# Performance work log

Hardware: AMD Instinct MI355X
Metric: run time of the kernel (lower is better)

Reference implementation:

```python
import jax, jax.numpy as jnp
import numpy as np

B, N, D, H = 4, 1024, 512, 8
DH = D // H  # per-head dim for V and for each of the two Q/K halves
LAM = 0.5


def setup_inputs() -> dict:
    key = jax.random.key(0)
    ks = jax.random.split(key, 7)
    s = 0.02
    return {
        "x": jax.random.normal(ks[0], (B, N, D), dtype=jnp.float32),
        "Wq": jax.random.normal(ks[1], (D, 2 * D), dtype=jnp.float32) * s,
        "bq": jax.random.normal(ks[2], (2 * D,), dtype=jnp.float32) * s,
        "Wk": jax.random.normal(ks[3], (D, 2 * D), dtype=jnp.float32) * s,
        "bk": jax.random.normal(ks[4], (2 * D,), dtype=jnp.float32) * s,
        "Wv": jax.random.normal(ks[5], (D, D), dtype=jnp.float32) * s,
        "bv": jax.random.normal(ks[6], (D,), dtype=jnp.float32) * s,
    }


def reference(x, Wq, bq, Wk, bk, Wv, bv):
    b, n, d = x.shape
    q = (x @ Wq + bq).reshape(b, n, H, 2 * DH).transpose(0, 2, 1, 3)  # [B,H,N,2*DH]
    k = (x @ Wk + bk).reshape(b, n, H, 2 * DH).transpose(0, 2, 1, 3)
    v = (x @ Wv + bv).reshape(b, n, H, DH).transpose(0, 2, 1, 3)      # [B,H,N,DH]
    q1, q2 = q[..., :DH], q[..., DH:]
    k1, k2 = k[..., :DH], k[..., DH:]
    scale = 1.0 / jnp.sqrt(jnp.float32(DH))
    a1 = jax.nn.softmax(jnp.einsum("bhqd,bhkd->bhqk", q1, k1) * scale, axis=-1)
    a2 = jax.nn.softmax(jnp.einsum("bhqd,bhkd->bhqk", q2, k2) * scale, axis=-1)
    attn = a1 - LAM * a2                                              # [B,H,N,N]
    out = jnp.einsum("bhqk,bhkd->bhqd", attn, v)                      # [B,H,N,DH]
    return out.transpose(0, 2, 1, 3).reshape(b, n, d)
```

## Files before the change

### kernel.cpp

```cpp
#include <hip/hip_runtime.h>
#include <hip/hip_bf16.h>

typedef unsigned short u16;
typedef short s16x8 __attribute__((ext_vector_type(8)));
typedef float f32x4 __attribute__((ext_vector_type(4)));

__device__ inline u16 f2bf(float f) {
  union { float f; unsigned int u; } v; v.f = f;
  unsigned int r = v.u + 0x7fffu + ((v.u >> 16) & 1u);
  return (u16)(r >> 16);
}

__global__ __launch_bounds__(256) void cast_x_kernel(const float* __restrict__ x,
                                                     u16* __restrict__ xb) {
  int i = (blockIdx.x * 256 + threadIdx.x) * 8;
  float4 a = *(const float4*)(x + i);
  float4 b = *(const float4*)(x + i + 4);
  s16x8 o;
  o[0] = (short)f2bf(a.x); o[1] = (short)f2bf(a.y);
  o[2] = (short)f2bf(a.z); o[3] = (short)f2bf(a.w);
  o[4] = (short)f2bf(b.x); o[5] = (short)f2bf(b.y);
  o[6] = (short)f2bf(b.z); o[7] = (short)f2bf(b.w);
  *(s16x8*)(xb + i) = o;
}

__global__ __launch_bounds__(256) void transpose_cast_w(const float* __restrict__ src, int C,
                                                        int rowoff, u16* __restrict__ wt) {
  __shared__ float tile[64][65];
  int j0 = blockIdx.x * 64, k0 = blockIdx.y * 64;
  int tx = threadIdx.x % 64, ty4 = threadIdx.x / 64;
#pragma unroll
  for (int p = 0; p < 16; ++p) {
    int r = p * 4 + ty4;
    tile[r][tx] = src[(size_t)(k0 + r) * C + j0 + tx];
  }
  __syncthreads();
#pragma unroll
  for (int p = 0; p < 16; ++p) {
    int r = p * 4 + ty4;
    wt[(size_t)(rowoff + j0 + r) * 512 + k0 + tx] = f2bf(tile[tx][r]);
  }
}

__global__ __launch_bounds__(256, 2) void gemm_qkv(const u16* __restrict__ xb, const u16* __restrict__ wt,
                                                   const float* __restrict__ bq, const float* __restrict__ bk,
                                                   const float* __restrict__ bv,
                                                   u16* __restrict__ qa, u16* __restrict__ ka,
                                                   u16* __restrict__ va) {
  __shared__ __align__(16) u16 As[128 * 72];
  __shared__ __align__(16) u16 Bs[128 * 72];
  int m0 = blockIdx.x * 128, j0 = blockIdx.y * 128;
  int tid = threadIdx.x;
  int w = tid >> 6, lane = tid & 63, quad = lane >> 4, l16 = lane & 15;
  int wr = (w >> 1) * 64, wc = (w & 1) * 64;

  f32x4 acc[4][4];
#pragma unroll
  for (int i = 0; i < 4; ++i)
#pragma unroll
    for (int j = 0; j < 4; ++j)
#pragma unroll
      for (int r = 0; r < 4; ++r) acc[i][j][r] = 0.f;

  for (int kk = 0; kk < 8; ++kk) {
    int k0 = kk * 64;
    __syncthreads();
#pragma unroll
    for (int i = 0; i < 4; ++i) {
      int c = tid * 4 + i;
      int row = c >> 3, cc = c & 7;
      *(int4*)(&As[row * 72 + cc * 8]) = *(const int4*)(xb + (size_t)(m0 + row) * 512 + k0 + cc * 8);
      *(int4*)(&Bs[row * 72 + cc * 8]) = *(const int4*)(wt + (size_t)(j0 + row) * 512 + k0 + cc * 8);
    }
    __syncthreads();
#pragma unroll
    for (int kb = 0; kb < 2; ++kb) {
      s16x8 af[4], bf[4];
#pragma unroll
      for (int rb = 0; rb < 4; ++rb)
        af[rb] = *(const s16x8*)(&As[(wr + rb * 16 + l16) * 72 + kb * 32 + quad * 8]);
#pragma unroll
      for (int cb = 0; cb < 4; ++cb)
        bf[cb] = *(const s16x8*)(&Bs[(wc + cb * 16 + l16) * 72 + kb * 32 + quad * 8]);
#pragma unroll
      for (int rb = 0; rb < 4; ++rb)
#pragma unroll
        for (int cb = 0; cb < 4; ++cb)
          acc[rb][cb] = __builtin_amdgcn_mfma_f32_16x16x32_bf16(af[rb], bf[cb], acc[rb][cb], 0, 0, 0);
    }
  }

#pragma unroll
  for (int cb = 0; cb < 4; ++cb) {
    int j = j0 + wc + cb * 16 + l16;
    float bias = (j < 1024) ? bq[j] : (j < 2048) ? bk[j - 1024] : bv[j - 2048];
#pragma unroll
    for (int rb = 0; rb < 4; ++rb) {
#pragma unroll
      for (int r = 0; r < 4; ++r) {
        int m = m0 + wr + rb * 16 + quad * 4 + r;
        int bidx = m >> 10, n = m & 1023;
        u16 o = f2bf(acc[rb][cb][r] + bias);
        if (j < 1024) {
          int h = j >> 7, r2 = j & 127;
          qa[((size_t)((bidx * 8 + h) * 1024 + n)) * 128 + r2] = o;
        } else if (j < 2048) {
          int jj = j - 1024, h = jj >> 7, r2 = jj & 127;
          ka[((size_t)((bidx * 8 + h) * 1024 + n)) * 128 + r2] = o;
        } else {
          int jj = j - 2048, h = jj >> 6, d = jj & 63;
          va[((size_t)((bidx * 8 + h) * 64 + d)) * 1024 + n] = o;
        }
      }
    }
  }
}

__global__ __launch_bounds__(256, 2) void attn_kernel(const u16* __restrict__ qa, const u16* __restrict__ ka,
                                                      const u16* __restrict__ va, float* __restrict__ out) {
  __shared__ __align__(16) u16 Ks[64 * 136];
  __shared__ __align__(16) u16 Vs[64 * 72];
  __shared__ __align__(16) u16 Ps[64 * 72];
  int bh = blockIdx.x, b = bh >> 3, h = bh & 7;
  int q0 = blockIdx.y * 64;
  int tid = threadIdx.x, w = tid >> 6, lane = tid & 63, quad = lane >> 4, l16 = lane & 15;

  const u16* qrow = qa + (size_t)(bh * 1024 + q0 + w * 16 + l16) * 128;
  s16x8 q1f[2], q2f[2];
  q1f[0] = *(const s16x8*)(qrow + quad * 8);
  q1f[1] = *(const s16x8*)(qrow + 32 + quad * 8);
  q2f[0] = *(const s16x8*)(qrow + 64 + quad * 8);
  q2f[1] = *(const s16x8*)(qrow + 96 + quad * 8);

  f32x4 O1[5], O2[5];
#pragma unroll
  for (int i = 0; i < 5; ++i)
#pragma unroll
    for (int r = 0; r < 4; ++r) { O1[i][r] = 0.f; O2[i][r] = 0.f; }

  s16x8 onesf;
#pragma unroll
  for (int i = 0; i < 8; ++i) onesf[i] = (l16 == 0) ? (short)0x3F80 : (short)0;

  for (int kt = 0; kt < 16; ++kt) {
    int n0 = kt * 64;
    __syncthreads();
#pragma unroll
    for (int i = 0; i < 4; ++i) {
      int c = tid * 4 + i, row = c >> 4, cc = c & 15;
      *(int4*)(&Ks[row * 136 + cc * 8]) = *(const int4*)(ka + (size_t)(bh * 1024 + n0 + row) * 128 + cc * 8);
    }
#pragma unroll
    for (int i = 0; i < 2; ++i) {
      int c = tid * 2 + i, row = c >> 3, cc = c & 7;
      *(int4*)(&Vs[row * 72 + cc * 8]) = *(const int4*)(va + (size_t)(bh * 64 + row) * 1024 + n0 + cc * 8);
    }
    __syncthreads();

    s16x8 vf[4][2];
#pragma unroll
    for (int ct = 0; ct < 4; ++ct)
#pragma unroll
      for (int kb = 0; kb < 2; ++kb)
        vf[ct][kb] = *(const s16x8*)(&Vs[(ct * 16 + l16) * 72 + kb * 32 + quad * 8]);

    {
#pragma unroll
      for (int nt = 0; nt < 4; ++nt) {
        f32x4 sv; sv[0] = sv[1] = sv[2] = sv[3] = 0.f;
#pragma unroll
        for (int kb = 0; kb < 2; ++kb) {
          s16x8 kf = *(const s16x8*)(&Ks[(nt * 16 + l16) * 136 + kb * 32 + quad * 8]);
          sv = __builtin_amdgcn_mfma_f32_16x16x32_bf16(q1f[kb], kf, sv, 0, 0, 0);
        }
#pragma unroll
        for (int r = 0; r < 4; ++r)
          Ps[(w * 16 + quad * 4 + r) * 72 + nt * 16 + l16] = f2bf(__expf(sv[r] * 0.125f));
      }
      asm volatile("s_waitcnt lgkmcnt(0)" ::: "memory");
      s16x8 pf0 = *(const s16x8*)(&Ps[(w * 16 + l16) * 72 + quad * 8]);
      s16x8 pf1 = *(const s16x8*)(&Ps[(w * 16 + l16) * 72 + 32 + quad * 8]);
#pragma unroll
      for (int ct = 0; ct < 5; ++ct) {
        s16x8 b0 = (ct < 4) ? vf[ct][0] : onesf;
        s16x8 b1 = (ct < 4) ? vf[ct][1] : onesf;
        O1[ct] = __builtin_amdgcn_mfma_f32_16x16x32_bf16(pf0, b0, O1[ct], 0, 0, 0);
        O1[ct] = __builtin_amdgcn_mfma_f32_16x16x32_bf16(pf1, b1, O1[ct], 0, 0, 0);
      }
      asm volatile("" ::: "memory");
    }
    {
#pragma unroll
      for (int nt = 0; nt < 4; ++nt) {
        f32x4 sv; sv[0] = sv[1] = sv[2] = sv[3] = 0.f;
#pragma unroll
        for (int kb = 0; kb < 2; ++kb) {
          s16x8 kf = *(const s16x8*)(&Ks[(nt * 16 + l16) * 136 + 64 + kb * 32 + quad * 8]);
          sv = __builtin_amdgcn_mfma_f32_16x16x32_bf16(q2f[kb], kf, sv, 0, 0, 0);
        }
#pragma unroll
        for (int r = 0; r < 4; ++r)
          Ps[(w * 16 + quad * 4 + r) * 72 + nt * 16 + l16] = f2bf(__expf(sv[r] * 0.125f));
      }
      asm volatile("s_waitcnt lgkmcnt(0)" ::: "memory");
      s16x8 pf0 = *(const s16x8*)(&Ps[(w * 16 + l16) * 72 + quad * 8]);
      s16x8 pf1 = *(const s16x8*)(&Ps[(w * 16 + l16) * 72 + 32 + quad * 8]);
#pragma unroll
      for (int ct = 0; ct < 5; ++ct) {
        s16x8 b0 = (ct < 4) ? vf[ct][0] : onesf;
        s16x8 b1 = (ct < 4) ? vf[ct][1] : onesf;
        O2[ct] = __builtin_amdgcn_mfma_f32_16x16x32_bf16(pf0, b0, O2[ct], 0, 0, 0);
        O2[ct] = __builtin_amdgcn_mfma_f32_16x16x32_bf16(pf1, b1, O2[ct], 0, 0, 0);
      }
      asm volatile("" ::: "memory");
    }
  }

  float inv1[4], inv2[4];
#pragma unroll
  for (int r = 0; r < 4; ++r) {
    float l1 = __shfl(O1[4][r], lane & 48, 64);
    float l2 = __shfl(O2[4][r], lane & 48, 64);
    inv1[r] = 1.0f / l1;
    inv2[r] = 1.0f / l2;
  }
  int nb = q0 + w * 16 + quad * 4;
#pragma unroll
  for (int ct = 0; ct < 4; ++ct)
#pragma unroll
    for (int r = 0; r < 4; ++r) {
      float val = O1[ct][r] * inv1[r] - 0.5f * O2[ct][r] * inv2[r];
      out[(size_t)(b * 1024 + nb + r) * 512 + h * 64 + ct * 16 + l16] = val;
    }
}

extern "C" void kernel_launch(void* const* d_in, const int* in_sizes, int n_in,
                              void* d_out, int out_size, void* d_ws, size_t ws_size,
                              hipStream_t stream) {
  (void)in_sizes; (void)n_in; (void)out_size; (void)ws_size;
  const float* x  = (const float*)d_in[0];
  const float* Wq = (const float*)d_in[1];
  const float* bq = (const float*)d_in[2];
  const float* Wk = (const float*)d_in[3];
  const float* bk = (const float*)d_in[4];
  const float* Wv = (const float*)d_in[5];
  const float* bv = (const float*)d_in[6];
  float* out = (float*)d_out;

  char* ws = (char*)d_ws;
  u16* xb = (u16*)(ws);
  u16* wt = (u16*)(ws + 4194304);
  u16* qa = (u16*)(ws + 6815744);
  u16* ka = (u16*)(ws + 15204352);
  u16* va = (u16*)(ws + 23592960);

  cast_x_kernel<<<1024, 256, 0, stream>>>(x, xb);
  transpose_cast_w<<<dim3(16, 8), 256, 0, stream>>>(Wq, 1024, 0, wt);
  transpose_cast_w<<<dim3(16, 8), 256, 0, stream>>>(Wk, 1024, 1024, wt);
  transpose_cast_w<<<dim3(8, 8), 256, 0, stream>>>(Wv, 512, 2048, wt);
  gemm_qkv<<<dim3(32, 20), 256, 0, stream>>>(xb, wt, bq, bk, bv, qa, ka, va);
  attn_kernel<<<dim3(32, 16), 256, 0, stream>>>(qa, ka, va, out);
}
```

Baseline: 159.3 us.

## Use direct global-to-LDS loads with XOR swizzle and double-buffer K/V tiles

Both the QKV GEMM and the attention kernel now fill shared memory with global_load_lds instead of register round-trips. The padded LDS layouts are replaced by an XOR-swizzled layout to avoid bank conflicts. The attention kernel double-buffers its K/V tiles so the next tile's load overlaps the current tile's compute, and it computes both score halves into separate P buffers before the PV MFMAs. The trade-off is more LDS per block and reliance on a barrier to cover completion of the async loads, which may need explicit vmcnt waits.

```diff
diff --git a/kernel.cpp b/kernel.cpp
--- a/kernel.cpp
+++ b/kernel.cpp
@@ -9,6 +9,11 @@
   union { float f; unsigned int u; } v; v.f = f;
   unsigned int r = v.u + 0x7fffu + ((v.u >> 16) & 1u);
   return (u16)(r >> 16);
+}
+
+__device__ __forceinline__ void g2lds16(const u16* g, u16* l) {
+  __builtin_amdgcn_global_load_lds((const __attribute__((address_space(1))) void*)g,
+                                   (__attribute__((address_space(3))) void*)l, 16, 0, 0);
 }
 
 __global__ __launch_bounds__(256) void cast_x_kernel(const float* __restrict__ x,
@@ -47,13 +52,22 @@
                                                    const float* __restrict__ bv,
                                                    u16* __restrict__ qa, u16* __restrict__ ka,
                                                    u16* __restrict__ va) {
-  __shared__ __align__(16) u16 As[128 * 72];
-  __shared__ __align__(16) u16 Bs[128 * 72];
+  __shared__ __align__(16) u16 As[128 * 64];
+  __shared__ __align__(16) u16 Bs[128 * 64];
   int m0 = blockIdx.x * 128, j0 = blockIdx.y * 128;
   int tid = threadIdx.x;
   int w = tid >> 6, lane = tid & 63, quad = lane >> 4, l16 = lane & 15;
   int wr = (w >> 1) * 64, wc = (w & 1) * 64;
 
+  int srow[4], scol[4], sbase[4];
+#pragma unroll
+  for (int it = 0; it < 4; ++it) {
+    int s = it * 256 + tid;
+    srow[it] = s >> 3;
+    scol[it] = (s & 7) ^ ((s >> 3) & 7);
+    sbase[it] = (s & ~63) * 8;
+  }
+
   f32x4 acc[4][4];
 #pragma unroll
   for (int i = 0; i < 4; ++i)
@@ -66,27 +80,29 @@
     int k0 = kk * 64;
     __syncthreads();
 #pragma unroll
-    for (int i = 0; i < 4; ++i) {
-      int c = tid * 4 + i;
-      int row = c >> 3, cc = c & 7;
-      *(int4*)(&As[row * 72 + cc * 8]) = *(const int4*)(xb + (size_t)(m0 + row) * 512 + k0 + cc * 8);
-      *(int4*)(&Bs[row * 72 + cc * 8]) = *(const int4*)(wt + (size_t)(j0 + row) * 512 + k0 + cc * 8);
+    for (int it = 0; it < 4; ++it) {
+      g2lds16(xb + (size_t)(m0 + srow[it]) * 512 + k0 + scol[it] * 8, &As[sbase[it]]);
+      g2lds16(wt + (size_t)(j0 + srow[it]) * 512 + k0 + scol[it] * 8, &Bs[sbase[it]]);
     }
     __syncthreads();
 #pragma unroll
     for (int kb = 0; kb < 2; ++kb) {
-      s16x8 af[4], bf[4];
+      s16x8 af[4], bfr[4];
+#pragma unroll
+      for (int rb = 0; rb < 4; ++rb) {
+        int row = wr + rb * 16 + l16;
+        af[rb] = *(const s16x8*)(&As[row * 64 + (((kb * 4 + quad) ^ (row & 7)) * 8)]);
+      }
+#pragma unroll
+      for (int cb = 0; cb < 4; ++cb) {
+        int row = wc + cb * 16 + l16;
+        bfr[cb] = *(const s16x8*)(&Bs[row * 64 + (((kb * 4 + quad) ^ (row & 7)) * 8)]);
+      }
 #pragma unroll
       for (int rb = 0; rb < 4; ++rb)
-        af[rb] = *(const s16x8*)(&As[(wr + rb * 16 + l16) * 72 + kb * 32 + quad * 8]);
-#pragma unroll
-      for (int cb = 0; cb < 4; ++cb)
-        bf[cb] = *(const s16x8*)(&Bs[(wc + cb * 16 + l16) * 72 + kb * 32 + quad * 8]);
-#pragma unroll
-      for (int rb = 0; rb < 4; ++rb)
 #pragma unroll
         for (int cb = 0; cb < 4; ++cb)
-          acc[rb][cb] = __builtin_amdgcn_mfma_f32_16x16x32_bf16(af[rb], bf[cb], acc[rb][cb], 0, 0, 0);
+          acc[rb][cb] = __builtin_amdgcn_mfma_f32_16x16x32_bf16(af[rb], bfr[cb], acc[rb][cb], 0, 0, 0);
     }
   }
 
@@ -118,19 +134,19 @@
 
 __global__ __launch_bounds__(256, 2) void attn_kernel(const u16* __restrict__ qa, const u16* __restrict__ ka,
                                                       const u16* __restrict__ va, float* __restrict__ out) {
-  __shared__ __align__(16) u16 Ks[64 * 136];
-  __shared__ __align__(16) u16 Vs[64 * 72];
-  __shared__ __align__(16) u16 Ps[64 * 72];
+  __shared__ __align__(16) u16 Ks[2][64 * 128];
+  __shared__ __align__(16) u16 Vs[2][64 * 64];
+  __shared__ __align__(16) u16 Ps[2][64 * 72];
   int bh = blockIdx.x, b = bh >> 3, h = bh & 7;
   int q0 = blockIdx.y * 64;
   int tid = threadIdx.x, w = tid >> 6, lane = tid & 63, quad = lane >> 4, l16 = lane & 15;
 
   const u16* qrow = qa + (size_t)(bh * 1024 + q0 + w * 16 + l16) * 128;
-  s16x8 q1f[2], q2f[2];
-  q1f[0] = *(const s16x8*)(qrow + quad * 8);
-  q1f[1] = *(const s16x8*)(qrow + 32 + quad * 8);
-  q2f[0] = *(const s16x8*)(qrow + 64 + quad * 8);
-  q2f[1] = *(const s16x8*)(qrow + 96 + quad * 8);
+  s16x8 qf[2][2];
+  qf[0][0] = *(const s16x8*)(qrow + quad * 8);
+  qf[0][1] = *(const s16x8*)(qrow + 32 + quad * 8);
+  qf[1][0] = *(const s16x8*)(qrow + 64 + quad * 8);
+  qf[1][1] = *(const s16x8*)(qrow + 96 + quad * 8);
 
   f32x4 O1[5], O2[5];
 #pragma unroll
@@ -142,78 +158,80 @@
 #pragma unroll
   for (int i = 0; i < 8; ++i) onesf[i] = (l16 == 0) ? (short)0x3F80 : (short)0;
 
+  int krow[4], kcol[4], kbse[4];
+#pragma unroll
+  for (int it = 0; it < 4; ++it) {
+    int s = it * 256 + tid;
+    krow[it] = s >> 4; kcol[it] = (s & 15) ^ ((s >> 4) & 7); kbse[it] = (s & ~63) * 8;
+  }
+  int vrow[2], vcol[2], vbse[2];
+#pragma unroll
+  for (int it = 0; it < 2; ++it) {
+    int s = it * 256 + tid;
+    vrow[it] = s >> 3; vcol[it] = (s & 7) ^ ((s >> 3) & 7); vbse[it] = (s & ~63) * 8;
+  }
+  const u16* kgbase = ka + (size_t)bh * 1024 * 128;
+  const u16* vgbase = va + (size_t)bh * 64 * 1024;
+
+  auto stage = [&](int kt, int bufi) {
+    int n0 = kt * 64;
+#pragma unroll
+    for (int it = 0; it < 4; ++it)
+      g2lds16(kgbase + (size_t)(n0 + krow[it]) * 128 + kcol[it] * 8, &Ks[bufi][kbse[it]]);
+#pragma unroll
+    for (int it = 0; it < 2; ++it)
+      g2lds16(vgbase + (size_t)vrow[it] * 1024 + n0 + vcol[it] * 8, &Vs[bufi][vbse[it]]);
+  };
+
+  stage(0, 0);
+  __syncthreads();
+
   for (int kt = 0; kt < 16; ++kt) {
-    int n0 = kt * 64;
-    __syncthreads();
-#pragma unroll
-    for (int i = 0; i < 4; ++i) {
-      int c = tid * 4 + i, row = c >> 4, cc = c & 15;
-      *(int4*)(&Ks[row * 136 + cc * 8]) = *(const int4*)(ka + (size_t)(bh * 1024 + n0 + row) * 128 + cc * 8);
-    }
-#pragma unroll
-    for (int i = 0; i < 2; ++i) {
-      int c = tid * 2 + i, row = c >> 3, cc = c & 7;
-      *(int4*)(&Vs[row * 72 + cc * 8]) = *(const int4*)(va + (size_t)(bh * 64 + row) * 1024 + n0 + cc * 8);
-    }
-    __syncthreads();
+    int cur = kt & 1;
+    if (kt < 15) stage(kt + 1, cur ^ 1);
 
     s16x8 vf[4][2];
 #pragma unroll
     for (int ct = 0; ct < 4; ++ct)
 #pragma unroll
-      for (int kb = 0; kb < 2; ++kb)
-        vf[ct][kb] = *(const s16x8*)(&Vs[(ct * 16 + l16) * 72 + kb * 32 + quad * 8]);
-
-    {
+      for (int kb = 0; kb < 2; ++kb) {
+        int row = ct * 16 + l16;
+        vf[ct][kb] = *(const s16x8*)(&Vs[cur][row * 64 + (((kb * 4 + quad) ^ (row & 7)) * 8)]);
+      }
+
+#pragma unroll
+    for (int hh = 0; hh < 2; ++hh) {
 #pragma unroll
       for (int nt = 0; nt < 4; ++nt) {
         f32x4 sv; sv[0] = sv[1] = sv[2] = sv[3] = 0.f;
 #pragma unroll
         for (int kb = 0; kb < 2; ++kb) {
-          s16x8 kf = *(const s16x8*)(&Ks[(nt * 16 + l16) * 136 + kb * 32 + quad * 8]);
-          sv = __builtin_amdgcn_mfma_f32_16x16x32_bf16(q1f[kb], kf, sv, 0, 0, 0);
+          int row = nt * 16 + l16;
+          s16x8 kf = *(const s16x8*)(&Ks[cur][row * 128 + (((hh * 8 + kb * 4 + quad) ^ (row & 7)) * 8)]);
+          sv = __builtin_amdgcn_mfma_f32_16x16x32_bf16(qf[hh][kb], kf, sv, 0, 0, 0);
         }
 #pragma unroll
         for (int r = 0; r < 4; ++r)
-          Ps[(w * 16 + quad * 4 + r) * 72 + nt * 16 + l16] = f2bf(__expf(sv[r] * 0.125f));
-      }
-      asm volatile("s_waitcnt lgkmcnt(0)" ::: "memory");
-      s16x8 pf0 = *(const s16x8*)(&Ps[(w * 16 + l16) * 72 + quad * 8]);
-      s16x8 pf1 = *(const s16x8*)(&Ps[(w * 16 + l16) * 72 + 32 + quad * 8]);
-#pragma unroll
-      for (int ct = 0; ct < 5; ++ct) {
-        s16x8 b0 = (ct < 4) ? vf[ct][0] : onesf;
-        s16x8 b1 = (ct < 4) ? vf[ct][1] : onesf;
-        O1[ct] = __builtin_amdgcn_mfma_f32_16x16x32_bf16(pf0, b0, O1[ct], 0, 0, 0);
-        O1[ct] = __builtin_amdgcn_mfma_f32_16x16x32_bf16(pf1, b1, O1[ct], 0, 0, 0);
-      }
-      asm volatile("" ::: "memory");
-    }
-    {
-#pragma unroll
-      for (int nt = 0; nt < 4; ++nt) {
-        f32x4 sv; sv[0] = sv[1] = sv[2] = sv[3] = 0.f;
-#pragma unroll
-        for (int kb = 0; kb < 2; ++kb) {
-          s16x8 kf = *(const s16x8*)(&Ks[(nt * 16 + l16) * 136 + 64 + kb * 32 + quad * 8]);
-          sv = __builtin_amdgcn_mfma_f32_16x16x32_bf16(q2f[kb], kf, sv, 0, 0, 0);
-        }
-#pragma unroll
-        for (int r = 0; r < 4; ++r)
-          Ps[(w * 16 + quad * 4 + r) * 72 + nt * 16 + l16] = f2bf(__expf(sv[r] * 0.125f));
-      }
-      asm volatile("s_waitcnt lgkmcnt(0)" ::: "memory");
-      s16x8 pf0 = *(const s16x8*)(&Ps[(w * 16 + l16) * 72 + quad * 8]);
-      s16x8 pf1 = *(const s16x8*)(&Ps[(w * 16 + l16) * 72 + 32 + quad * 8]);
-#pragma unroll
-      for (int ct = 0; ct < 5; ++ct) {
-        s16x8 b0 = (ct < 4) ? vf[ct][0] : onesf;
-        s16x8 b1 = (ct < 4) ? vf[ct][1] : onesf;
-        O2[ct] = __builtin_amdgcn_mfma_f32_16x16x32_bf16(pf0, b0, O2[ct], 0, 0, 0);
-        O2[ct] = __builtin_amdgcn_mfma_f32_16x16x32_bf16(pf1, b1, O2[ct], 0, 0, 0);
-      }
-      asm volatile("" ::: "memory");
-    }
+          Ps[hh][(w * 16 + quad * 4 + r) * 72 + nt * 16 + l16] = f2bf(__expf(sv[r] * 0.125f));
+      }
+    }
+    asm volatile("s_waitcnt lgkmcnt(0)" ::: "memory");
+    s16x8 pf[2][2];
+#pragma unroll
+    for (int hh = 0; hh < 2; ++hh) {
+      pf[hh][0] = *(const s16x8*)(&Ps[hh][(w * 16 + l16) * 72 + quad * 8]);
+      pf[hh][1] = *(const s16x8*)(&Ps[hh][(w * 16 + l16) * 72 + 32 + quad * 8]);
+    }
+#pragma unroll
+    for (int ct = 0; ct < 5; ++ct) {
+      s16x8 b0 = (ct < 4) ? vf[ct][0] : onesf;
+      s16x8 b1 = (ct < 4) ? vf[ct][1] : onesf;
+      O1[ct] = __builtin_amdgcn_mfma_f32_16x16x32_bf16(pf[0][0], b0, O1[ct], 0, 0, 0);
+      O1[ct] = __builtin_amdgcn_mfma_f32_16x16x32_bf16(pf[0][1], b1, O1[ct], 0, 0, 0);
+      O2[ct] = __builtin_amdgcn_mfma_f32_16x16x32_bf16(pf[1][0], b0, O2[ct], 0, 0, 0);
+      O2[ct] = __builtin_amdgcn_mfma_f32_16x16x32_bf16(pf[1][1], b1, O2[ct], 0, 0, 0);
+    }
+    __syncthreads();
   }
 
   float inv1[4], inv2[4];
```

New measurement: 139.2 us. 1.14x faster.
